# Optimization experiments

Measured on AMD Instinct MI355X. Metric: run time of the kernel, lower is better.

## Reference

```python
import jax, jax.numpy as jnp
import numpy as np

D = 768
HID = 4 * D
B = 16
HRES = 32
WRES = 32
T = HRES * WRES


def layernorm(x, g, b, eps=1e-5):
    m = jnp.mean(x, axis=-1, keepdims=True)
    v = jnp.mean(jnp.square(x - m), axis=-1, keepdims=True)
    return (x - m) * jax.lax.rsqrt(v + eps) * g + b


def q_shift(x, H, W):
    # Vision-RWKV quad-directional token shift: split channels into 4 groups,
    # each group takes the neighboring patch's value in one direction (zero pad).
    Bn, N, C = x.shape
    xi = x.reshape(Bn, H, W, C)
    c = C // 4
    g0 = jnp.pad(xi[:, :, :-1, 0 * c:1 * c], ((0, 0), (0, 0), (1, 0), (0, 0)))  # from left
    g1 = jnp.pad(xi[:, :, 1:, 1 * c:2 * c], ((0, 0), (0, 0), (0, 1), (0, 0)))   # from right
    g2 = jnp.pad(xi[:, :-1, :, 2 * c:3 * c], ((0, 0), (1, 0), (0, 0), (0, 0)))  # from above
    g3 = jnp.pad(xi[:, 1:, :, 3 * c:4 * c], ((0, 0), (0, 1), (0, 0), (0, 0)))   # from below
    return jnp.concatenate([g0, g1, g2, g3], axis=-1).reshape(Bn, N, C)


def wkv_scan(w_log, u, k, v):
    # Numerically stable RWKV WKV recurrence (per-channel linear attention).
    # k, v: [B, T, C]; w = -exp(w_log) is the per-channel decay, u the bonus.
    w = -jnp.exp(w_log)
    kT = jnp.swapaxes(k, 0, 1)  # [T, B, C]
    vT = jnp.swapaxes(v, 0, 1)
    Bn, C = k.shape[0], k.shape[2]
    aa0 = jnp.zeros((Bn, C), k.dtype)
    bb0 = jnp.zeros((Bn, C), k.dtype)
    pp0 = jnp.full((Bn, C), -1e30, k.dtype)

    def step(carry, kv):
        aa, bb, pp = carry
        kt, vt = kv
        ww = u + kt
        p = jnp.maximum(pp, ww)
        e1 = jnp.exp(pp - p)
        e2 = jnp.exp(ww - p)
        out = (e1 * aa + e2 * vt) / (e1 * bb + e2)
        ww2 = pp + w
        p2 = jnp.maximum(ww2, kt)
        e1b = jnp.exp(ww2 - p2)
        e2b = jnp.exp(kt - p2)
        return (e1b * aa + e2b * vt, e1b * bb + e2b, p2), out

    _, outT = jax.lax.scan(step, (aa0, bb0, pp0), (kT, vT))
    return jnp.swapaxes(outT, 0, 1)  # [B, T, C]


def setup_inputs() -> dict:
    key = jax.random.key(0)
    ks = jax.random.split(key, 16)

    def nrm(k, shape, s=0.02):
        return jax.random.normal(k, shape, jnp.float32) * s

    return {
        "x": jax.random.normal(ks[0], (B, T, D), jnp.float32),
        "H": HRES,
        "W": WRES,
        "ln1_g": jnp.ones((D,), jnp.float32),
        "ln1_b": jnp.zeros((D,), jnp.float32),
        "ln2_g": jnp.ones((D,), jnp.float32),
        "ln2_b": jnp.zeros((D,), jnp.float32),
        "mu_k": jax.random.uniform(ks[1], (D,), jnp.float32),
        "mu_v": jax.random.uniform(ks[2], (D,), jnp.float32),
        "mu_r": jax.random.uniform(ks[3], (D,), jnp.float32),
        "w_log": nrm(ks[4], (D,), 0.5),
        "u": nrm(ks[5], (D,), 0.5),
        "Wk": nrm(ks[6], (D, D)),
        "Wv": nrm(ks[7], (D, D)),
        "Wr": nrm(ks[8], (D, D)),
        "Wo": nrm(ks[9], (D, D)),
        "cmu_k": jax.random.uniform(ks[10], (D,), jnp.float32),
        "cmu_r": jax.random.uniform(ks[11], (D,), jnp.float32),
        "Ck": nrm(ks[12], (HID, D)),
        "Cv": nrm(ks[13], (D, HID)),
        "Cr": nrm(ks[14], (D, D)),
    }


def reference(x, H, W, ln1_g, ln1_b, ln2_g, ln2_b, mu_k, mu_v, mu_r, w_log, u,
              Wk, Wv, Wr, Wo, cmu_k, cmu_r, Ck, Cv, Cr):
    h = x
    # ---- spatial mix (RWKV time-mix over patch sequence) ----
    a = layernorm(h, ln1_g, ln1_b)
    sx = q_shift(a, H, W)
    xk = a * mu_k + sx * (1.0 - mu_k)
    xv = a * mu_v + sx * (1.0 - mu_v)
    xr = a * mu_r + sx * (1.0 - mu_r)
    k = xk @ Wk.T
    v = xv @ Wv.T
    r = jax.nn.sigmoid(xr @ Wr.T)
    wkv = wkv_scan(w_log, u, k, v)
    h = h + (r * wkv) @ Wo.T
    # ---- channel mix (squared-ReLU gated FFN) ----
    a2 = layernorm(h, ln2_g, ln2_b)
    sx2 = q_shift(a2, H, W)
    xk2 = a2 * cmu_k + sx2 * (1.0 - cmu_k)
    xr2 = a2 * cmu_r + sx2 * (1.0 - cmu_r)
    kk = jnp.square(jax.nn.relu(xk2 @ Ck.T))
    h = h + jax.nn.sigmoid(xr2 @ Cr.T) * (kk @ Cv.T)
    # ---- outer residual from RWKVBlock.forward ----
    return h + x
```

## Files before the change

### kernel.cpp

```cpp
#include <hip/hip_runtime.h>
#include <hip/hip_bf16.h>

#define DD   768
#define TT   1024
#define BBATCH 16
#define NROWS (BBATCH * TT)
#define HIDN 3072
#define HHALF 1536
#define HH 32
#define WW 32
#define DW  (DD * DD)
#define DH  (DD * HIDN)
#define CCH 64
#define PCH (TT / CCH)

typedef float  floatx4 __attribute__((ext_vector_type(4)));
typedef __bf16 bf16x8  __attribute__((ext_vector_type(8)));

__device__ __forceinline__ float bf2f(__hip_bfloat16 v) { return __bfloat162float(v); }
__device__ __forceinline__ __hip_bfloat16 f2bf(float v) { return __float2bfloat16(v); }
__device__ __forceinline__ float toF(__hip_bfloat16 v) { return __bfloat162float(v); }
__device__ __forceinline__ float toF(float v) { return v; }

__global__ __launch_bounds__(256)
void cvt_k(const float* __restrict__ s, __hip_bfloat16* __restrict__ d, int n)
{
    const int i = (blockIdx.x * 256 + threadIdx.x) * 4;
    if (i >= n) return;
    const float4 v = *reinterpret_cast<const float4*>(s + i);
    __hip_bfloat16 o[4] = {f2bf(v.x), f2bf(v.y), f2bf(v.z), f2bf(v.w)};
    *reinterpret_cast<ushort4*>(d + i) = *reinterpret_cast<const ushort4*>(o);
}

template <typename TIN>
__global__ __launch_bounds__(256)
void ln_stats_k(const TIN* __restrict__ x,
                float* __restrict__ mean, float* __restrict__ rstd)
{
    const int row = blockIdx.x, tid = threadIdx.x;
    const int lane = tid & 63, wid = tid >> 6;
    const TIN* xr = x + (size_t)row * DD;
    float s1 = 0.f, s2 = 0.f;
#pragma unroll
    for (int i = 0; i < 3; ++i) {
        const float v = toF(xr[tid + i * 256]);
        s1 += v; s2 += v * v;
    }
#pragma unroll
    for (int off = 32; off > 0; off >>= 1) {
        s1 += __shfl_down(s1, off);
        s2 += __shfl_down(s2, off);
    }
    __shared__ float sh[8];
    if (lane == 0) { sh[wid] = s1; sh[4 + wid] = s2; }
    __syncthreads();
    if (tid == 0) {
        s1 = sh[0] + sh[1] + sh[2] + sh[3];
        s2 = sh[4] + sh[5] + sh[6] + sh[7];
        const float m = s1 * (1.f / DD);
        mean[row] = m;
        rstd[row] = rsqrtf(s2 * (1.f / DD) - m * m + 1e-5f);
    }
}

template <typename TIN>
__device__ __forceinline__ float ln_at(const TIN* __restrict__ x,
                                       const float* __restrict__ mean,
                                       const float* __restrict__ rstd,
                                       const float* __restrict__ g,
                                       const float* __restrict__ b,
                                       int grow, int c)
{
    return (toF(x[(size_t)grow * DD + c]) - mean[grow]) * rstd[grow] * g[c] + b[c];
}

template <typename TIN, int NOUT>
__global__ __launch_bounds__(256)
void mix_k(const TIN* __restrict__ x,
           const float* __restrict__ mean, const float* __restrict__ rstd,
           const float* __restrict__ g, const float* __restrict__ b,
           const float* __restrict__ muk,
           const float* __restrict__ muv,
           const float* __restrict__ mur,
           __hip_bfloat16* __restrict__ xk,
           __hip_bfloat16* __restrict__ xv,
           __hip_bfloat16* __restrict__ xr)
{
    const size_t idx = (size_t)blockIdx.x * 256 + threadIdx.x;
    const int c  = (int)(idx % DD);
    const int n  = (int)((idx / DD) % TT);
    const int bb = (int)(idx / ((size_t)DD * TT));
    const int y = n >> 5, xp = n & 31;
    const int grow = bb * TT + n;

    const float av = ln_at(x, mean, rstd, g, b, grow, c);

    const int grp = c / (DD / 4);
    int ny = y, nx = xp; bool ok;
    if      (grp == 0) { nx = xp - 1; ok = xp > 0;      }
    else if (grp == 1) { nx = xp + 1; ok = xp < WW - 1; }
    else if (grp == 2) { ny = y - 1;  ok = y > 0;       }
    else               { ny = y + 1;  ok = y < HH - 1;  }
    const float sx = ok ? ln_at(x, mean, rstd, g, b, bb * TT + ny * WW + nx, c) : 0.f;

    const float mk = muk[c], mr = mur[c];
    xk[idx] = f2bf(av * mk + sx * (1.f - mk));
    xr[idx] = f2bf(av * mr + sx * (1.f - mr));
    if (NOUT == 3) {
        const float mv = muv[c];
        xv[idx] = f2bf(av * mv + sx * (1.f - mv));
    }
}

#define BM 128
#define BN 128
#define BKK 64
#define LSTR 72

template <int MODE>
__global__ __launch_bounds__(256, 2)
void gemm_bt(const __hip_bfloat16* __restrict__ A,
             const __hip_bfloat16* __restrict__ W,
             int K, int Wstr, int Nn,
             __hip_bfloat16* __restrict__ outB,
             float* __restrict__ outF,
             const __hip_bfloat16* __restrict__ auxS,
             const __hip_bfloat16* __restrict__ auxH,
             const float* __restrict__ auxX)
{
    __shared__ __align__(16) unsigned short lA[BM * LSTR];
    __shared__ __align__(16) unsigned short lB[BN * LSTR];

    const int tid  = threadIdx.x;
    const int bm   = blockIdx.x, bn = blockIdx.y;
    const int lane = tid & 63, wid = tid >> 6;
    const int l15  = lane & 15, quad = lane >> 4;
    const int m0   = (wid & 1) * 64;
    const int n0   = (wid >> 1) * 64;

    floatx4 acc[4][4];
#pragma unroll
    for (int i = 0; i < 4; ++i)
#pragma unroll
        for (int j = 0; j < 4; ++j)
            acc[i][j] = floatx4{0.f, 0.f, 0.f, 0.f};

    for (int k0 = 0; k0 < K; k0 += BKK) {
#pragma unroll
        for (int it = 0; it < 4; ++it) {
            const int chunk = tid + it * 256;
            const int r  = chunk >> 3;
            const int c8 = chunk & 7;
            const uint4 va = *reinterpret_cast<const uint4*>(
                A + (size_t)(bm * BM + r) * K + k0 + c8 * 8);
            const uint4 vb = *reinterpret_cast<const uint4*>(
                W + (size_t)(bn * BN + r) * Wstr + k0 + c8 * 8);
            *reinterpret_cast<uint4*>(&lA[r * LSTR + c8 * 8]) = va;
            *reinterpret_cast<uint4*>(&lB[r * LSTR + c8 * 8]) = vb;
        }
        __syncthreads();
#pragma unroll
        for (int kk = 0; kk < BKK; kk += 32) {
            bf16x8 af[4], bfr[4];
#pragma unroll
            for (int i = 0; i < 4; ++i)
                af[i] = *reinterpret_cast<const bf16x8*>(
                    &lA[(m0 + i * 16 + l15) * LSTR + kk + quad * 8]);
#pragma unroll
            for (int j = 0; j < 4; ++j)
                bfr[j] = *reinterpret_cast<const bf16x8*>(
                    &lB[(n0 + j * 16 + l15) * LSTR + kk + quad * 8]);
#pragma unroll
            for (int i = 0; i < 4; ++i)
#pragma unroll
                for (int j = 0; j < 4; ++j)
                    acc[i][j] = __builtin_amdgcn_mfma_f32_16x16x32_bf16(
                        af[i], bfr[j], acc[i][j], 0, 0, 0);
        }
        __syncthreads();
    }

#pragma unroll
    for (int i = 0; i < 4; ++i) {
#pragma unroll
        for (int j = 0; j < 4; ++j) {
#pragma unroll
            for (int r = 0; r < 4; ++r) {
                const int grow = bm * BM + m0 + i * 16 + quad * 4 + r;
                const int gcol = bn * BN + n0 + j * 16 + l15;
                const size_t idx = (size_t)grow * Nn + gcol;
                const float v = acc[i][j][r];
                if (MODE == 0) {
                    outB[idx] = f2bf(v);
                } else if (MODE == 1) {
                    outB[idx] = f2bf(1.f / (1.f + __expf(-v)));
                } else if (MODE == 2) {
                    outB[idx] = f2bf(v + auxX[idx]);
                } else if (MODE == 3) {
                    const float t = fmaxf(v, 0.f);
                    outB[idx] = f2bf(t * t);
                } else if (MODE == 4) {
                    outF[idx] = bf2f(auxH[idx]) + bf2f(auxS[idx]) * v + auxX[idx];
                } else {
                    outF[idx] += bf2f(auxS[idx]) * v;
                }
            }
        }
    }
}

__global__ __launch_bounds__(256)
void wkv_passA(const float* __restrict__ w_log,
               const __hip_bfloat16* __restrict__ k,
               const __hip_bfloat16* __restrict__ v,
               float* __restrict__ SA, float* __restrict__ SB,
               float* __restrict__ SP)
{
    const int c  = blockIdx.x * 256 + threadIdx.x;
    const int j  = blockIdx.y;
    const int bb = blockIdx.z;
    const float w = -__expf(w_log[c]);
    const size_t base = ((size_t)bb * TT + j * CCH) * DD + c;
    float a = 0.f, b = 0.f, p = -1e30f;
#pragma unroll 4
    for (int t = 0; t < CCH; ++t) {
        const size_t o = base + (size_t)t * DD;
        const float kt = bf2f(k[o]);
        const float vt = bf2f(v[o]);
        const float ww2 = p + w;
        const float p2  = fmaxf(ww2, kt);
        const float e1  = __expf(ww2 - p2);
        const float e2  = __expf(kt - p2);
        a = e1 * a + e2 * vt;
        b = e1 * b + e2;
        p = p2;
    }
    const size_t si = ((size_t)bb * PCH + j) * DD + c;
    SA[si] = a; SB[si] = b; SP[si] = p;
}

__global__ __launch_bounds__(256)
void wkv_scanj(const float* __restrict__ w_log,
               float* __restrict__ SA, float* __restrict__ SB,
               float* __restrict__ SP)
{
    const int idx = blockIdx.x * 256 + threadIdx.x;
    const int c = idx % DD, bb = idx / DD;
    const float wC = -__expf(w_log[c]) * (float)CCH;
    float a = 0.f, b = 0.f, p = -1e30f;
#pragma unroll
    for (int j = 0; j < PCH; ++j) {
        const size_t si = ((size_t)bb * PCH + j) * DD + c;
        const float aj = SA[si], bj = SB[si], pj = SP[si];
        SA[si] = a; SB[si] = b; SP[si] = p;
        const float pd = p + wC;
        const float pn = fmaxf(pd, pj);
        const float e1 = __expf(pd - pn);
        const float e2 = __expf(pj - pn);
        a = e1 * a + e2 * aj;
        b = e1 * b + e2 * bj;
        p = pn;
    }
}

__global__ __launch_bounds__(256)
void wkv_passB(const float* __restrict__ w_log, const float* __restrict__ u,
               const __hip_bfloat16* __restrict__ k,
               const __hip_bfloat16* __restrict__ v,
               const __hip_bfloat16* __restrict__ r,
               __hip_bfloat16* __restrict__ rw,
               const float* __restrict__ SA, const float* __restrict__ SB,
               const float* __restrict__ SP)
{
    const int c  = blockIdx.x * 256 + threadIdx.x;
    const int j  = blockIdx.y;
    const int bb = blockIdx.z;
    const float w  = -__expf(w_log[c]);
    const float uu = u[c];
    const size_t si = ((size_t)bb * PCH + j) * DD + c;
    float aa = SA[si], bbv = SB[si], pp = SP[si];
    const size_t base = ((size_t)bb * TT + j * CCH) * DD + c;
#pragma unroll 4
    for (int t = 0; t < CCH; ++t) {
        const size_t o = base + (size_t)t * DD;
        const float kt = bf2f(k[o]);
        const float vt = bf2f(v[o]);
        const float rt = bf2f(r[o]);
        const float ww = uu + kt;
        const float p  = fmaxf(pp, ww);
        const float e1 = __expf(pp - p);
        const float e2 = __expf(ww - p);
        const float ov = __fdividef(e1 * aa + e2 * vt, e1 * bbv + e2);
        rw[o] = f2bf(rt * ov);
        const float ww2 = pp + w;
        const float p2  = fmaxf(ww2, kt);
        const float e1b = __expf(ww2 - p2);
        const float e2b = __expf(kt - p2);
        aa  = e1b * aa + e2b * vt;
        bbv = e1b * bbv + e2b;
        pp  = p2;
    }
}

extern "C" void kernel_launch(void* const* d_in, const int* in_sizes, int n_in,
                              void* d_out, int out_size, void* d_ws, size_t ws_size,
                              hipStream_t stream)
{
    (void)in_sizes; (void)n_in; (void)out_size;
    const float* x     = (const float*)d_in[0];
    const float* ln1_g = (const float*)d_in[3];
    const float* ln1_b = (const float*)d_in[4];
    const float* ln2_g = (const float*)d_in[5];
    const float* ln2_b = (const float*)d_in[6];
    const float* mu_k  = (const float*)d_in[7];
    const float* mu_v  = (const float*)d_in[8];
    const float* mu_r  = (const float*)d_in[9];
    const float* w_log = (const float*)d_in[10];
    const float* u     = (const float*)d_in[11];
    const float* Wk    = (const float*)d_in[12];
    const float* Wv    = (const float*)d_in[13];
    const float* Wr    = (const float*)d_in[14];
    const float* Wo    = (const float*)d_in[15];
    const float* cmu_k = (const float*)d_in[16];
    const float* cmu_r = (const float*)d_in[17];
    const float* Ck    = (const float*)d_in[18];
    const float* Cv    = (const float*)d_in[19];
    const float* Cr    = (const float*)d_in[20];
    float* out = (float*)d_out;

    const size_t ND = (size_t)NROWS * DD;
    const size_t SL = ND * 2;
    const size_t WBYTES = (size_t)(5 * DW + 2 * DH) * 2;
    const size_t NSTATE = (size_t)BBATCH * PCH * DD;
    const size_t NEED = 5 * SL + WBYTES
                      + 2 * (size_t)NROWS * sizeof(float)
                      + 3 * NSTATE * sizeof(float);
    if (ws_size < NEED) return;

    char* w = (char*)d_ws;
    __hip_bfloat16* S0 = (__hip_bfloat16*)(w);
    __hip_bfloat16* S1 = (__hip_bfloat16*)(w + 1 * SL);
    __hip_bfloat16* S2 = (__hip_bfloat16*)(w + 2 * SL);
    __hip_bfloat16* S3 = (__hip_bfloat16*)(w + 3 * SL);
    __hip_bfloat16* S4 = (__hip_bfloat16*)(w + 4 * SL);
    __hip_bfloat16* WkB = (__hip_bfloat16*)(w + 5 * SL);
    __hip_bfloat16* WvB = WkB + DW;
    __hip_bfloat16* WrB = WvB + DW;
    __hip_bfloat16* WoB = WrB + DW;
    __hip_bfloat16* CrB = WoB + DW;
    __hip_bfloat16* CkB = CrB + DW;
    __hip_bfloat16* CvB = CkB + DH;
    float* meanB = (float*)(w + 5 * SL + WBYTES);
    float* rstdB = meanB + NROWS;
    float* SAb = rstdB + NROWS;
    float* SBb = SAb + NSTATE;
    float* SPb = SBb + NSTATE;

    const int EW_GRID = (int)(ND / 256);
    const dim3 g768(NROWS / BM, DD / BN);
    const dim3 g1536(NROWS / BM, HHALF / BN);
    const dim3 gwkv(DD / 256, PCH, BBATCH);
    const int CB_W = DW / 4 / 256;
    const int CB_H = DH / 4 / 256;

    cvt_k<<<CB_W, 256, 0, stream>>>(Wk, WkB, DW);
    cvt_k<<<CB_W, 256, 0, stream>>>(Wv, WvB, DW);
    cvt_k<<<CB_W, 256, 0, stream>>>(Wr, WrB, DW);
    cvt_k<<<CB_W, 256, 0, stream>>>(Wo, WoB, DW);
    cvt_k<<<CB_W, 256, 0, stream>>>(Cr, CrB, DW);
    cvt_k<<<CB_H, 256, 0, stream>>>(Ck, CkB, DH);
    cvt_k<<<CB_H, 256, 0, stream>>>(Cv, CvB, DH);

    ln_stats_k<float><<<NROWS, 256, 0, stream>>>(x, meanB, rstdB);
    mix_k<float, 3><<<EW_GRID, 256, 0, stream>>>(x, meanB, rstdB, ln1_g, ln1_b,
                                                 mu_k, mu_v, mu_r, S0, S1, S2);
    gemm_bt<0><<<g768, 256, 0, stream>>>(S0, WkB, DD, DD, DD, S3, nullptr, nullptr, nullptr, nullptr);
    gemm_bt<0><<<g768, 256, 0, stream>>>(S1, WvB, DD, DD, DD, S4, nullptr, nullptr, nullptr, nullptr);
    gemm_bt<1><<<g768, 256, 0, stream>>>(S2, WrB, DD, DD, DD, S0, nullptr, nullptr, nullptr, nullptr);
    wkv_passA<<<gwkv, 256, 0, stream>>>(w_log, S3, S4, SAb, SBb, SPb);
    wkv_scanj<<<(BBATCH * DD) / 256, 256, 0, stream>>>(w_log, SAb, SBb, SPb);
    wkv_passB<<<gwkv, 256, 0, stream>>>(w_log, u, S3, S4, S0, S1, SAb, SBb, SPb);
    gemm_bt<2><<<g768, 256, 0, stream>>>(S1, WoB, DD, DD, DD, S2, nullptr, nullptr, nullptr, x);

    ln_stats_k<__hip_bfloat16><<<NROWS, 256, 0, stream>>>(S2, meanB, rstdB);
    mix_k<__hip_bfloat16, 2><<<EW_GRID, 256, 0, stream>>>(S2, meanB, rstdB, ln2_g, ln2_b,
                                                          cmu_k, nullptr, cmu_r, S0, nullptr, S3);
    gemm_bt<1><<<g768, 256, 0, stream>>>(S3, CrB, DD, DD, DD, S1, nullptr, nullptr, nullptr, nullptr);
    __hip_bfloat16* kk = S3;
    gemm_bt<3><<<g1536, 256, 0, stream>>>(S0, CkB, DD, DD, HHALF,
                                          kk, nullptr, nullptr, nullptr, nullptr);
    gemm_bt<4><<<g768, 256, 0, stream>>>(kk, CvB, HHALF, HIDN, DD,
                                         nullptr, out, S1, S2, x);
    gemm_bt<3><<<g1536, 256, 0, stream>>>(S0, CkB + (size_t)HHALF * DD, DD, DD, HHALF,
                                          kk, nullptr, nullptr, nullptr, nullptr);
    gemm_bt<5><<<g768, 256, 0, stream>>>(kk, CvB + HHALF, HHALF, HIDN, DD,
                                         nullptr, out, S1, nullptr, nullptr);
}
```

Baseline: 627.5 us.

## Load GEMM tiles directly into LDS with XOR-swizzled layout

Replaces the register-staged global-to-LDS copy in the bf16 GEMM with global_load_lds direct transfers of 16 bytes per lane. The padded LDS stride is replaced by an XOR swizzle on 8-element column groups, applied both when loading and when reading MFMA fragments, so bank conflicts are avoided without padding. This removes the VGPR round trip and reduces LDS footprint. The risk is that the 16-byte global_load_lds variant and the swizzle mapping must match the hardware's lane-to-LDS placement exactly, or results will be wrong.

New measurement: 614.8 us. -2.0%, faster.

```diff
diff --git a/kernel.cpp b/kernel.cpp
--- a/kernel.cpp
+++ b/kernel.cpp
@@ -22,6 +22,10 @@
 __device__ __forceinline__ float toF(__hip_bfloat16 v) { return __bfloat162float(v); }
 __device__ __forceinline__ float toF(float v) { return v; }
 
+#define GL2LDS(gp, lp)  __builtin_amdgcn_global_load_lds(                     \
+    (const __attribute__((address_space(1))) void*)(gp),                      \
+    (__attribute__((address_space(3))) void*)(lp), 16, 0, 0)
+
 __global__ __launch_bounds__(256)
 void cvt_k(const float* __restrict__ s, __hip_bfloat16* __restrict__ d, int n)
 {
@@ -115,7 +119,6 @@
 #define BM 128
 #define BN 128
 #define BKK 64
-#define LSTR 72
 
 template <int MODE>
 __global__ __launch_bounds__(256, 2)
@@ -128,8 +131,8 @@
              const __hip_bfloat16* __restrict__ auxH,
              const float* __restrict__ auxX)
 {
-    __shared__ __align__(16) unsigned short lA[BM * LSTR];
-    __shared__ __align__(16) unsigned short lB[BN * LSTR];
+    __shared__ __align__(16) unsigned short lA[BM * BKK];
+    __shared__ __align__(16) unsigned short lB[BN * BKK];
 
     const int tid  = threadIdx.x;
     const int bm   = blockIdx.x, bn = blockIdx.y;
@@ -138,6 +141,10 @@
     const int m0   = (wid & 1) * 64;
     const int n0   = (wid >> 1) * 64;
 
+    const int srow  = lane >> 3;
+    const int gcolg = (lane & 7) ^ (srow & 7);
+    const int s0    = wid * 4;
+
     floatx4 acc[4][4];
 #pragma unroll
     for (int i = 0; i < 4; ++i)
@@ -145,31 +152,31 @@
         for (int j = 0; j < 4; ++j)
             acc[i][j] = floatx4{0.f, 0.f, 0.f, 0.f};
 
+    const int swzbase = l15 & 7;
+
     for (int k0 = 0; k0 < K; k0 += BKK) {
 #pragma unroll
-        for (int it = 0; it < 4; ++it) {
-            const int chunk = tid + it * 256;
-            const int r  = chunk >> 3;
-            const int c8 = chunk & 7;
-            const uint4 va = *reinterpret_cast<const uint4*>(
-                A + (size_t)(bm * BM + r) * K + k0 + c8 * 8);
-            const uint4 vb = *reinterpret_cast<const uint4*>(
-                W + (size_t)(bn * BN + r) * Wstr + k0 + c8 * 8);
-            *reinterpret_cast<uint4*>(&lA[r * LSTR + c8 * 8]) = va;
-            *reinterpret_cast<uint4*>(&lB[r * LSTR + c8 * 8]) = vb;
+        for (int t = 0; t < 4; ++t) {
+            const int s   = s0 + t;
+            const int row = s * 8 + srow;
+            GL2LDS(A + (size_t)(bm * BM + row) * K    + k0 + gcolg * 8,
+                   &lA[s * 512]);
+            GL2LDS(W + (size_t)(bn * BN + row) * Wstr + k0 + gcolg * 8,
+                   &lB[s * 512]);
         }
         __syncthreads();
 #pragma unroll
         for (int kk = 0; kk < BKK; kk += 32) {
+            const int swz = (((kk >> 3) + quad) ^ swzbase) * 8;
             bf16x8 af[4], bfr[4];
 #pragma unroll
             for (int i = 0; i < 4; ++i)
                 af[i] = *reinterpret_cast<const bf16x8*>(
-                    &lA[(m0 + i * 16 + l15) * LSTR + kk + quad * 8]);
+                    &lA[(m0 + i * 16 + l15) * BKK + swz]);
 #pragma unroll
             for (int j = 0; j < 4; ++j)
                 bfr[j] = *reinterpret_cast<const bf16x8*>(
-                    &lB[(n0 + j * 16 + l15) * LSTR + kk + quad * 8]);
+                    &lB[(n0 + j * 16 + l15) * BKK + swz]);
 #pragma unroll
             for (int i = 0; i < 4; ++i)
 #pragma unroll
```
